# Optimization experiments

Hardware: AMD Instinct MI355X
Metric: run time of the kernel (lower is better)

Reference implementation:

```python
import jax, jax.numpy as jnp
import numpy as np

B, N, D, H, DK, DV, E = 32, 512, 128, 8, 16, 16, 128
MLP_H = 16


def _uniform(key, shape, fan):
    s = 1.0 / np.sqrt(fan)
    return jax.random.uniform(key, shape, jnp.float32, -s, s)


def setup_inputs() -> dict:
    key = jax.random.key(0)
    ks = jax.random.split(key, 13)
    q = jax.random.normal(ks[0], (B, N, D), jnp.float32)
    mask = jax.random.randint(ks[1], (B, N, N), 0, 2) > 0  # True = attention not allowed
    edge_matrix = jax.random.normal(ks[2], (B, N, N), jnp.float32)
    # per-head projection weights (init: uniform(-1/sqrt(last_dim), ...))
    W_query = _uniform(ks[3], (H, D, DK), DK)
    W_key = _uniform(ks[4], (H, D, DK), DK)
    W_val = _uniform(ks[5], (H, D, DV), DV)
    W_out = _uniform(ks[6], (H, DV, E), E)
    # edge MLP: 1 -> 16 -> 16 -> n_heads, ReLU between layers
    mlp_W1 = _uniform(ks[7], (1, MLP_H), 1)
    mlp_b1 = _uniform(ks[8], (MLP_H,), 1)
    mlp_W2 = _uniform(ks[9], (MLP_H, MLP_H), MLP_H)
    mlp_b2 = _uniform(ks[10], (MLP_H,), MLP_H)
    mlp_W3 = _uniform(ks[11], (MLP_H, H), MLP_H)
    mlp_b3 = _uniform(ks[12], (H,), MLP_H)
    return dict(q=q, mask=mask, edge_matrix=edge_matrix,
                W_query=W_query, W_key=W_key, W_val=W_val, W_out=W_out,
                mlp_W1=mlp_W1, mlp_b1=mlp_b1, mlp_W2=mlp_W2, mlp_b2=mlp_b2,
                mlp_W3=mlp_W3, mlp_b3=mlp_b3)


def reference(q, mask, edge_matrix, W_query, W_key, W_val, W_out,
              mlp_W1, mlp_b1, mlp_W2, mlp_b2, mlp_W3, mlp_b3):
    dk = W_query.shape[-1]
    norm = 1.0 / np.sqrt(dk)
    # per-head projections: [H,B,N,dk]
    Q = jnp.einsum('bni,hid->hbnd', q, W_query)
    K = jnp.einsum('bni,hid->hbnd', q, W_key)
    V = jnp.einsum('bni,hid->hbnd', q, W_val)
    # scaled QK^T: [H,B,N,N]
    comp = norm * jnp.einsum('hbqd,hbkd->hbqk', Q, K)
    # edge-bias MLP on each scalar edge weight: [B,N,N,1] -> [B,N,N,H]
    e = edge_matrix[..., None]
    h1 = jax.nn.relu(e @ mlp_W1 + mlp_b1)
    h2 = jax.nn.relu(h1 @ mlp_W2 + mlp_b2)
    bias = h2 @ mlp_W3 + mlp_b3
    comp = comp + jnp.transpose(bias, (3, 0, 1, 2))
    # masked softmax (mask True = disallowed)
    m = mask[None]  # broadcast over heads
    comp = jnp.where(m, -jnp.inf, comp)
    attn = jax.nn.softmax(comp, axis=-1)
    attn = jnp.where(m, 0.0, attn)
    heads = jnp.einsum('hbqk,hbkd->hbqd', attn, V)  # [H,B,N,dv]
    out = jnp.einsum('hbqd,hde->bqe', heads, W_out)  # [B,N,E]
    return out
```

## Files before the change

### kernel.cpp

```cpp
#include <hip/hip_runtime.h>
#include <hip/hip_bf16.h>
#include <float.h>

#define Bc 32
#define Nc 512
#define Dc 128
#define Hc 8
#define DKc 16
#define Ec 128
#define LOG2E 1.44269504088896340736f
#define SCLAMP 80.0f

typedef __attribute__((ext_vector_type(4))) short s16x4;
typedef __attribute__((ext_vector_type(8))) short s16x8;
typedef __attribute__((ext_vector_type(4))) float f32x4;

union BFU { __hip_bfloat16 b; short s; };
static __device__ inline short f2bf(float f) { BFU u; u.b = __float2bfloat16(f); return u.s; }

static __device__ inline unsigned rnd16(float x) { return __float_as_uint(x) + 0x8000u; }
static __device__ inline s16x4 pack4(float a, float b, float c, float d) {
  union { unsigned u[2]; s16x4 v; } r;
  r.u[0] = __builtin_amdgcn_perm(rnd16(b), rnd16(a), 0x07060302u);
  r.u[1] = __builtin_amdgcn_perm(rnd16(d), rnd16(c), 0x07060302u);
  return r.v;
}

#if __has_builtin(__builtin_amdgcn_exp2f)
#define EXP2F(x) __builtin_amdgcn_exp2f(x)
#else
#define EXP2F(x) exp2f(x)
#endif

static __device__ inline f32x4 mfma16(s16x4 a, s16x4 b, f32x4 c) {
#if __has_builtin(__builtin_amdgcn_mfma_f32_16x16x16bf16_1k)
  return __builtin_amdgcn_mfma_f32_16x16x16bf16_1k(a, b, c, 0, 0, 0);
#else
  int lane = threadIdx.x & 63;
  int g = lane >> 4, base = lane & 15;
  int src0 = (base + 32 * g) & 63;
  int src1 = (base + 32 * g + 16) & 63;
  int ax = ((int*)&a)[0], ay = ((int*)&a)[1];
  int bx = ((int*)&b)[0], by = ((int*)&b)[1];
  int A0 = __shfl(ax, src0), A1 = __shfl(ay, src0);
  int A2 = __shfl(ax, src1), A3 = __shfl(ay, src1);
  int B0 = __shfl(bx, src0), B1 = __shfl(by, src0);
  int B2 = __shfl(bx, src1), B3 = __shfl(by, src1);
  if (g >= 2) { A0 = A1 = A2 = A3 = 0; B0 = B1 = B2 = B3 = 0; }
  s16x8 A8, B8;
  ((int*)&A8)[0] = A0; ((int*)&A8)[1] = A1; ((int*)&A8)[2] = A2; ((int*)&A8)[3] = A3;
  ((int*)&B8)[0] = B0; ((int*)&B8)[1] = B1; ((int*)&B8)[2] = B2; ((int*)&B8)[3] = B3;
  return __builtin_amdgcn_mfma_f32_16x16x32_bf16(A8, B8, c, 0, 0, 0);
#endif
}

__global__ __launch_bounds__(256) void prep_kernel(
    const float* __restrict__ Wq, const float* __restrict__ Wk, const float* __restrict__ Wv,
    const float* __restrict__ Wo,
    const unsigned char* __restrict__ m, int* __restrict__ flag,
    short* __restrict__ Wt, short* __restrict__ Wob)
{
  int blk = blockIdx.x;
  int t = threadIdx.x;
  if (blk == 256) {
    __shared__ int red[4];
    int any = 0;
    for (int u = t; u < 16384; u += 256)
      if ((u & 3) != 0 && m[u] != 0) any = 1;
    unsigned long long bal = __ballot(any != 0);
    if ((t & 63) == 0) red[t >> 6] = (bal != 0ULL) ? 1 : 0;
    __syncthreads();
    if (t == 0) *flag = red[0] | red[1] | red[2] | red[3];
    return;
  }
  int o = blk * 256 + t;
  if (o < 49152) {
    int mat = o >> 14, r = o & 16383;
    int hk = r >> 7, d = r & 127;
    const float* src = (mat == 0) ? Wq : ((mat == 1) ? Wk : Wv);
    Wt[o] = f2bf(src[(hk >> 4) * 2048 + d * 16 + (hk & 15)]);
  } else {
    int o2 = o - 49152;
    int et = o2 >> 11, s = (o2 >> 8) & 7, lane = (o2 >> 2) & 63, i = o2 & 3;
    Wob[o2] = f2bf(Wo[(s * 16 + (lane >> 4) * 4 + i) * 128 + et * 16 + (lane & 15)]);
  }
}

__global__ __launch_bounds__(256, 4) void qkv4(
    const float* __restrict__ q, const short* __restrict__ Wt,
    short* __restrict__ Qb, short* __restrict__ Kb, short* __restrict__ Vt)
{
  __shared__ short qs[16][136];
  int blk = blockIdx.x;
  int b = blk >> 5;
  int rt = (blk & 31) << 4;
  int t = threadIdx.x;
  int wid = t >> 6, lane = t & 63;
  int lq = lane & 15, lg = lane >> 4;

  #pragma unroll
  for (int it = 0; it < 2; ++it) {
    int u = t + it * 256;
    int row = u >> 5, c4 = (u & 31) << 2;
    float4 v = *(const float4*)&q[((((b << 9) + rt + row) << 7)) + c4];
    *(s16x4*)&qs[row][c4] = pack4(v.x, v.y, v.z, v.w);
  }
  __syncthreads();

  s16x4 af[8];
  #pragma unroll
  for (int ks = 0; ks < 8; ++ks)
    af[ks] = *(const s16x4*)&qs[lq][ks * 16 + lg * 4];

  #pragma unroll 1
  for (int pj = 0; pj < 3; ++pj) {
    const short* Wm = Wt + pj * 16384;
    #pragma unroll
    for (int c2 = 0; c2 < 2; ++c2) {
      int ct = wid * 2 + c2;
      f32x4 acc = (f32x4)0.f;
      #pragma unroll
      for (int ks = 0; ks < 8; ++ks) {
        s16x4 bf = *(const s16x4*)&Wm[(ct * 16 + lq) * 128 + ks * 16 + lg * 4];
        acc = mfma16(af[ks], bf, acc);
      }
      if (pj == 0) {
        s16x4 pk = pack4(acc[0] * (0.25f * LOG2E), acc[1] * (0.25f * LOG2E),
                         acc[2] * (0.25f * LOG2E), acc[3] * (0.25f * LOG2E));
        #pragma unroll
        for (int r = 0; r < 4; ++r)
          Qb[(ct << 18) + (b << 13) + ((rt + lg * 4 + r) << 4) + lq] = pk[r];
      } else if (pj == 1) {
        s16x4 pk = pack4(acc[0], acc[1], acc[2], acc[3]);
        #pragma unroll
        for (int r = 0; r < 4; ++r)
          Kb[(ct << 18) + (b << 13) + ((rt + lg * 4 + r) << 4) + lq] = pk[r];
      } else {
        s16x4 pk = pack4(acc[0], acc[1], acc[2], acc[3]);
        *(s16x4*)&Vt[(ct << 18) + (((b << 4) + lq) << 9) + rt + lg * 4] = pk;
      }
    }
  }
}

__global__ __launch_bounds__(256, 4) void attn6(
    const float* __restrict__ edge, const unsigned char* __restrict__ maskB,
    const int* __restrict__ flag,
    const short* __restrict__ Qb, const short* __restrict__ Kb, const short* __restrict__ Vt,
    const short* __restrict__ Wob,
    const float* __restrict__ mW1, const float* __restrict__ mb1,
    const float* __restrict__ mW2, const float* __restrict__ mb2,
    const float* __restrict__ mW3, const float* __restrict__ mb3,
    float* __restrict__ out)
{
  __shared__ __align__(16) char smem[36864];

  int t = threadIdx.x;
  int wid = t >> 6, lane = t & 63;
  int lq = lane & 15, lg = lane >> 4;
  int b = blockIdx.x >> 5;
  int qt = (blockIdx.x & 31) << 4;
  int mflag = *flag;

  short* bias_w = (short*)(smem + wid * 5120);
  float (*etile)[16] = (float(*)[16])(smem + 20480 + wid * 1024);
  float* d2L = (float*)smem;
  float* psL = (float*)(smem + 34816);

  float W1v[4], b1v[4];
  f32x4 b2v, b3v;
  s16x4 w2f, w3f;
  #pragma unroll
  for (int i = 0; i < 4; ++i) {
    int v = lg * 4 + i;
    W1v[i] = mW1[v];
    b1v[i] = mb1[v];
    b2v[i] = mb2[v];
    b3v[i] = (v < 8) ? mb3[v] * LOG2E : 0.f;
    w2f[i] = f2bf(mW2[v * 16 + lq]);
    w3f[i] = (lq < 8) ? f2bf(mW3[v * 8 + lq] * LOG2E) : (short)0;
  }

  const short* Kl = Kb + (b << 13) + (lq << 4) + (lg << 2);
  const short* Vl = Vt + (((b << 4) + lq) << 9) + (lg << 2);
  const short* Ql = Qb + (b << 13) + ((qt + lq) << 4) + (lg << 2);
  unsigned ebase = (((b << 9) + qt + (lane >> 2)) << 9) + (lane & 3) * 4;
  unsigned mbase = (((b << 9) + qt + lq) << 9) + (lg << 2);

  s16x4 qf[8];
  #pragma unroll
  for (int h = 0; h < 8; ++h) qf[h] = *(const s16x4*)(Ql + (h << 18));

  f32x4 oacc[8];
  float psum[8];
  #pragma unroll
  for (int h = 0; h < 8; ++h) { oacc[h] = (f32x4)0.f; psum[h] = 0.f; }

  int jb = wid << 4;
  float4 ev = *(const float4*)&edge[ebase + jb];
  int4 mkv;
  if (mflag) {
    uchar4 u = *(const uchar4*)&maskB[mbase + jb];
    mkv.x = u.x; mkv.y = u.y; mkv.z = u.z; mkv.w = u.w;
  } else {
    mkv = *(const int4*)&((const int*)maskB)[mbase + jb];
  }

  #pragma unroll 1
  for (int cc = 0; cc < 8; ++cc) {
    jb = ((cc << 2) | wid) << 4;
    *(float4*)&etile[lane >> 2][(lane & 3) * 4] = ev;

    float4 evn; int4 mkn;
    if (cc < 7) {
      int jbn = (((cc + 1) << 2) | wid) << 4;
      evn = *(const float4*)&edge[ebase + jbn];
      if (mflag) {
        uchar4 u = *(const uchar4*)&maskB[mbase + jbn];
        mkn.x = u.x; mkn.y = u.y; mkn.z = u.z; mkn.w = u.w;
      } else {
        mkn = *(const int4*)&((const int*)maskB)[mbase + jbn];
      }
    } else { evn = ev; mkn = mkv; }

    s16x4 kf[8];
    #pragma unroll
    for (int h = 0; h < 8; ++h) kf[h] = *(const s16x4*)(Kl + (h << 18) + (jb << 4));

    #pragma unroll 4
    for (int qq = 0; qq < 16; ++qq) {
      float e = etile[qq][lq];
      s16x4 h1f = pack4(fmaxf(0.f, fmaf(e, W1v[0], b1v[0])),
                        fmaxf(0.f, fmaf(e, W1v[1], b1v[1])),
                        fmaxf(0.f, fmaf(e, W1v[2], b1v[2])),
                        fmaxf(0.f, fmaf(e, W1v[3], b1v[3])));
      f32x4 c2 = mfma16(w2f, h1f, b2v);
      s16x4 rf = pack4(fmaxf(c2[0], 0.f), fmaxf(c2[1], 0.f),
                       fmaxf(c2[2], 0.f), fmaxf(c2[3], 0.f));
      f32x4 c3 = mfma16(w3f, rf, b3v);
      if (lg < 2) {
        s16x4 pk = pack4(c3[0], c3[1], c3[2], c3[3]);
        #pragma unroll
        for (int r = 0; r < 4; ++r)
          bias_w[(lg * 4 + r) * 320 + qq * 20 + lq] = pk[r];
      }
    }

    #pragma unroll
    for (int h = 0; h < 8; ++h) {
      union { s16x4 v; int i[2]; } bb;
      bb.v = *(const s16x4*)&bias_w[h * 320 + lq * 20 + lg * 4];
      f32x4 sc;
      sc[0] = __int_as_float(bb.i[0] << 16);
      sc[1] = __int_as_float(bb.i[0] & 0xffff0000);
      sc[2] = __int_as_float(bb.i[1] << 16);
      sc[3] = __int_as_float(bb.i[1] & 0xffff0000);
      sc = mfma16(kf[h], qf[h], sc);
      s16x4 vf = *(const s16x4*)(Vl + (h << 18) + jb);
      float p0 = mkv.x ? 0.f : EXP2F(fminf(sc[0], SCLAMP));
      float p1 = mkv.y ? 0.f : EXP2F(fminf(sc[1], SCLAMP));
      float p2 = mkv.z ? 0.f : EXP2F(fminf(sc[2], SCLAMP));
      float p3 = mkv.w ? 0.f : EXP2F(fminf(sc[3], SCLAMP));
      psum[h] += (p0 + p1) + (p2 + p3);
      s16x4 pf = pack4(p0, p1, p2, p3);
      oacc[h] = mfma16(vf, pf, oacc[h]);
    }
    ev = evn; mkv = mkn;
  }

  #pragma unroll
  for (int h = 0; h < 8; ++h) {
    float s = psum[h];
    s += __shfl_xor(s, 16);
    s += __shfl_xor(s, 32);
    psum[h] = s;
  }
  if (lg == 0) {
    #pragma unroll
    for (int h = 0; h < 8; ++h) psL[wid * 128 + h * 16 + lq] = psum[h];
  }
  __syncthreads();

  s16x4 obf[8];
  #pragma unroll
  for (int h = 0; h < 8; ++h) {
    float tot = psL[h * 16 + lq] + psL[128 + h * 16 + lq]
              + psL[256 + h * 16 + lq] + psL[384 + h * 16 + lq];
    float inv = (tot > 0.f) ? 1.f / tot : 0.f;
    obf[h] = pack4(oacc[h][0] * inv, oacc[h][1] * inv, oacc[h][2] * inv, oacc[h][3] * inv);
  }

  f32x4 d2a[8];
  #pragma unroll
  for (int et = 0; et < 8; ++et) d2a[et] = (f32x4)0.f;
  #pragma unroll
  for (int s = 0; s < 8; ++s) {
    #pragma unroll
    for (int et = 0; et < 8; ++et) {
      s16x4 wo = *(const s16x4*)&Wob[((et * 8 + s) << 8) + (lane << 2)];
      d2a[et] = mfma16(wo, obf[s], d2a[et]);
    }
  }

  #pragma unroll
  for (int et = 0; et < 8; ++et)
    #pragma unroll
    for (int r = 0; r < 4; ++r)
      d2L[(wid * 128 + et * 16 + lg * 4 + r) * 17 + lq] = d2a[et][r];
  __syncthreads();

  #pragma unroll
  for (int k = 0; k < 2; ++k) {
    int et = wid * 2 + k;
    #pragma unroll
    for (int r = 0; r < 4; ++r) {
      int el = (et * 16 + lg * 4 + r) * 17 + lq;
      float v = d2L[el] + d2L[2176 + el] + d2L[4352 + el] + d2L[6528 + el];
      out[(((b << 9) + qt + lq) << 7) + et * 16 + lg * 4 + r] = v;
    }
  }
}

extern "C" void kernel_launch(void* const* d_in, const int* in_sizes, int n_in,
                              void* d_out, int out_size, void* d_ws, size_t ws_size,
                              hipStream_t stream)
{
  const float* q    = (const float*)d_in[0];
  const unsigned char* mask = (const unsigned char*)d_in[1];
  const float* edge = (const float*)d_in[2];
  const float* Wq   = (const float*)d_in[3];
  const float* Wk   = (const float*)d_in[4];
  const float* Wv   = (const float*)d_in[5];
  const float* Wo   = (const float*)d_in[6];
  const float* mW1  = (const float*)d_in[7];
  const float* mb1  = (const float*)d_in[8];
  const float* mW2  = (const float*)d_in[9];
  const float* mb2  = (const float*)d_in[10];
  const float* mW3  = (const float*)d_in[11];
  const float* mb3  = (const float*)d_in[12];
  float* out = (float*)d_out;

  size_t per = (size_t)Hc * Bc * Nc * DKc;
  short* Wt  = (short*)d_ws;
  short* Wob = Wt + 49152;
  short* Qb  = Wob + 16384;
  short* Kb  = Qb + per;
  short* Vt  = Kb + per;
  int* flag  = (int*)(Vt + per);

  prep_kernel<<<dim3(257), dim3(256), 0, stream>>>(Wq, Wk, Wv, Wo, mask, flag, Wt, Wob);
  qkv4<<<dim3(Bc * 32), dim3(256), 0, stream>>>(q, Wt, Qb, Kb, Vt);
  attn6<<<dim3(Bc * 32), dim3(256), 0, stream>>>(edge, mask, flag, Qb, Kb, Vt, Wob,
      mW1, mb1, mW2, mb2, mW3, mb3, out);
}
```

Baseline: 124.2 us.

## Replace per-element edge MLP with exact piecewise-linear lookup table

The scalar-input ReLU edge MLP is an exact piecewise-linear function of the edge weight. A new prep block finds its breakpoints (first-layer and second-layer ReLU knots), sorts them, and stores a slope and intercept per segment and head. The attention kernel now copies this table into shared memory, binary-searches each edge value's segment, and gets each head's bias with one FMA, replacing the per-tile MFMA-based MLP evaluation and its bias staging in shared memory. The trade-off is dependent shared-memory lookups with scattered access patterns, and pack4 now uses a library bf16 conversion instead of the manual bit-twiddling path.

```diff
diff --git a/kernel.cpp b/kernel.cpp
--- a/kernel.cpp
+++ b/kernel.cpp
@@ -10,6 +10,7 @@
 #define Ec 128
 #define LOG2E 1.44269504088896340736f
 #define SCLAMP 80.0f
+#define KPAD 3.0e38f
 
 typedef __attribute__((ext_vector_type(4))) short s16x4;
 typedef __attribute__((ext_vector_type(8))) short s16x8;
@@ -17,13 +18,8 @@
 
 union BFU { __hip_bfloat16 b; short s; };
 static __device__ inline short f2bf(float f) { BFU u; u.b = __float2bfloat16(f); return u.s; }
-
-static __device__ inline unsigned rnd16(float x) { return __float_as_uint(x) + 0x8000u; }
 static __device__ inline s16x4 pack4(float a, float b, float c, float d) {
-  union { unsigned u[2]; s16x4 v; } r;
-  r.u[0] = __builtin_amdgcn_perm(rnd16(b), rnd16(a), 0x07060302u);
-  r.u[1] = __builtin_amdgcn_perm(rnd16(d), rnd16(c), 0x07060302u);
-  return r.v;
+  s16x4 r; r[0] = f2bf(a); r[1] = f2bf(b); r[2] = f2bf(c); r[3] = f2bf(d); return r;
 }
 
 #if __has_builtin(__builtin_amdgcn_exp2f)
@@ -54,14 +50,49 @@
 #endif
 }
 
+static __device__ __forceinline__ void h2pre_eval(
+    float e, const float* W1, const float* B1, const float* W2, const float* B2,
+    float* h2)
+{
+  float h1[16];
+  #pragma unroll
+  for (int u = 0; u < 16; ++u) h1[u] = fmaxf(0.f, fmaf(e, W1[u], B1[u]));
+  #pragma unroll
+  for (int v = 0; v < 16; ++v) {
+    float a = B2[v];
+    #pragma unroll
+    for (int u = 0; u < 16; ++u) a = fmaf(h1[u], W2[u * 16 + v], a);
+    h2[v] = a;
+  }
+}
+static __device__ __forceinline__ void bias_eval(
+    float e, const float* W1, const float* B1, const float* W2, const float* B2,
+    const float* W3, const float* B3, float* bias8)
+{
+  float h2[16];
+  h2pre_eval(e, W1, B1, W2, B2, h2);
+  #pragma unroll
+  for (int h = 0; h < 8; ++h) {
+    float a = B3[h];
+    #pragma unroll
+    for (int v = 0; v < 16; ++v) a = fmaf(fmaxf(h2[v], 0.f), W3[v * 8 + h], a);
+    bias8[h] = a;
+  }
+}
+
 __global__ __launch_bounds__(256) void prep_kernel(
     const float* __restrict__ Wq, const float* __restrict__ Wk, const float* __restrict__ Wv,
     const float* __restrict__ Wo,
     const unsigned char* __restrict__ m, int* __restrict__ flag,
-    short* __restrict__ Wt, short* __restrict__ Wob)
+    short* __restrict__ Wt, short* __restrict__ Wob,
+    const float* __restrict__ mW1, const float* __restrict__ mb1,
+    const float* __restrict__ mW2, const float* __restrict__ mb2,
+    const float* __restrict__ mW3, const float* __restrict__ mb3,
+    float* __restrict__ knotsG, float* __restrict__ coeffG)
 {
   int blk = blockIdx.x;
   int t = threadIdx.x;
+
   if (blk == 256) {
     __shared__ int red[4];
     int any = 0;
@@ -73,6 +104,111 @@
     if (t == 0) *flag = red[0] | red[1] | red[2] | red[3];
     return;
   }
+
+  if (blk == 257) {
+    __shared__ float t1raw[16], t1s[16];
+    __shared__ float ks[512], ks2[512];
+    __shared__ int cnt, n1s;
+
+    if (t < 16) {
+      float w = mW1[t];
+      t1raw[t] = (w != 0.f) ? (-mb1[t] / w) : KPAD;
+    }
+    for (int u = t; u < 512; u += 256) { ks[u] = KPAD; ks2[u] = KPAD; }
+    __syncthreads();
+    if (t < 16) {
+      float v = t1raw[t];
+      int r = 0;
+      #pragma unroll
+      for (int j = 0; j < 16; ++j) {
+        float vj = t1raw[j];
+        r += (vj < v) || (vj == v && j < t);
+      }
+      t1s[r] = v;
+    }
+    __syncthreads();
+    if (t == 0) {
+      int n1 = 0;
+      while (n1 < 16 && t1s[n1] < 1.0e37f) { ks[n1] = t1s[n1]; n1++; }
+      n1s = n1;
+      cnt = n1;
+    }
+    __syncthreads();
+    int n1 = n1s;
+    if (t <= n1) {
+      bool first = (t == 0), last = (t == n1);
+      float L = first ? 0.f : t1s[t - 1];
+      float R = last ? 0.f : t1s[t];
+      float p1, p2;
+      bool ok = true;
+      if (first && last) { p1 = 0.f; p2 = 1.f; }
+      else if (first)    { p1 = R - 1.f; p2 = R - 0.5f; }
+      else if (last)     { p1 = L + 0.5f; p2 = L + 1.f; }
+      else {
+        float w = R - L;
+        if (w > 0.f) { p1 = L + 0.25f * w; p2 = L + 0.75f * w; }
+        else ok = false;
+      }
+      if (ok && p2 > p1) {
+        float h2a[16], h2b[16];
+        h2pre_eval(p1, mW1, mb1, mW2, mb2, h2a);
+        h2pre_eval(p2, mW1, mb1, mW2, mb2, h2b);
+        #pragma unroll
+        for (int v = 0; v < 16; ++v) {
+          float bet = (h2b[v] - h2a[v]) / (p2 - p1);
+          float alp = fmaf(-bet, p1, h2a[v]);
+          float x = -alp / bet;
+          bool fin = (x == x) && (fabsf(x) < 1.0e37f) && (bet != 0.f);
+          bool inr = (first || x > L) && (last || x < R);
+          if (fin && inr) { int id = atomicAdd(&cnt, 1); ks[id] = x; }
+        }
+      }
+    }
+    __syncthreads();
+    int mknots = cnt;
+    for (int i = t; i < mknots; i += 256) {
+      float v = ks[i];
+      int r = 0;
+      for (int j = 0; j < mknots; ++j) {
+        float vj = ks[j];
+        r += (vj < v) || (vj == v && j < i);
+      }
+      ks2[r] = v;
+    }
+    __syncthreads();
+    for (int u = t; u < 512; u += 256) knotsG[u] = ks2[u];
+    for (int s = t; s < mknots + 1; s += 256) {
+      bool first = (s == 0), last = (s == mknots);
+      float L = first ? 0.f : ks2[s - 1];
+      float R = last ? 0.f : ks2[s];
+      float p1, p2;
+      if (first && last) { p1 = 0.f; p2 = 1.f; }
+      else if (first)    { p1 = R - 1.f; p2 = R - 0.5f; }
+      else if (last)     { p1 = L + 0.5f; p2 = L + 1.f; }
+      else { float w = R - L; p1 = L + 0.25f * w; p2 = L + 0.75f * w; }
+      float ba[8];
+      bias_eval(p1, mW1, mb1, mW2, mb2, mW3, mb3, ba);
+      if (p2 > p1) {
+        float bb[8];
+        bias_eval(p2, mW1, mb1, mW2, mb2, mW3, mb3, bb);
+        #pragma unroll
+        for (int h = 0; h < 8; ++h) {
+          float sl = (bb[h] - ba[h]) / (p2 - p1);
+          float c0 = fmaf(-sl, p1, ba[h]);
+          coeffG[h * 640 + s * 2]     = sl * LOG2E;
+          coeffG[h * 640 + s * 2 + 1] = c0 * LOG2E;
+        }
+      } else {
+        #pragma unroll
+        for (int h = 0; h < 8; ++h) {
+          coeffG[h * 640 + s * 2]     = 0.f;
+          coeffG[h * 640 + s * 2 + 1] = ba[h] * LOG2E;
+        }
+      }
+    }
+    return;
+  }
+
   int o = blk * 256 + t;
   if (o < 49152) {
     int mat = o >> 14, r = o & 16383;
@@ -143,14 +279,20 @@
   }
 }
 
-__global__ __launch_bounds__(256, 4) void attn6(
+static __device__ __forceinline__ int segof(const float* knotsL, float e) {
+  int p = 0;
+  #pragma unroll
+  for (int s = 256; s > 0; s >>= 1)
+    p += (knotsL[p + s - 1] <= e) ? s : 0;
+  return p;
+}
+
+__global__ __launch_bounds__(256, 4) void attn7(
     const float* __restrict__ edge, const unsigned char* __restrict__ maskB,
     const int* __restrict__ flag,
     const short* __restrict__ Qb, const short* __restrict__ Kb, const short* __restrict__ Vt,
     const short* __restrict__ Wob,
-    const float* __restrict__ mW1, const float* __restrict__ mb1,
-    const float* __restrict__ mW2, const float* __restrict__ mb2,
-    const float* __restrict__ mW3, const float* __restrict__ mb3,
+    const float* __restrict__ knotsG, const float* __restrict__ coeffG,
     float* __restrict__ out)
 {
   __shared__ __align__(16) char smem[36864];
@@ -162,29 +304,17 @@
   int qt = (blockIdx.x & 31) << 4;
   int mflag = *flag;
 
-  short* bias_w = (short*)(smem + wid * 5120);
-  float (*etile)[16] = (float(*)[16])(smem + 20480 + wid * 1024);
+  float* knotsL = (float*)smem;
+  float* coeffL = (float*)(smem + 2048);
   float* d2L = (float*)smem;
   float* psL = (float*)(smem + 34816);
 
-  float W1v[4], b1v[4];
-  f32x4 b2v, b3v;
-  s16x4 w2f, w3f;
-  #pragma unroll
-  for (int i = 0; i < 4; ++i) {
-    int v = lg * 4 + i;
-    W1v[i] = mW1[v];
-    b1v[i] = mb1[v];
-    b2v[i] = mb2[v];
-    b3v[i] = (v < 8) ? mb3[v] * LOG2E : 0.f;
-    w2f[i] = f2bf(mW2[v * 16 + lq]);
-    w3f[i] = (lq < 8) ? f2bf(mW3[v * 8 + lq] * LOG2E) : (short)0;
-  }
+  for (int u = t; u < 1408; u += 256)
+    ((float4*)smem)[u] = ((const float4*)knotsG)[u];
 
   const short* Kl = Kb + (b << 13) + (lq << 4) + (lg << 2);
   const short* Vl = Vt + (((b << 4) + lq) << 9) + (lg << 2);
   const short* Ql = Qb + (b << 13) + ((qt + lq) << 4) + (lg << 2);
-  unsigned ebase = (((b << 9) + qt + (lane >> 2)) << 9) + (lane & 3) * 4;
   unsigned mbase = (((b << 9) + qt + lq) << 9) + (lg << 2);
 
   s16x4 qf[8];
@@ -197,7 +327,7 @@
   for (int h = 0; h < 8; ++h) { oacc[h] = (f32x4)0.f; psum[h] = 0.f; }
 
   int jb = wid << 4;
-  float4 ev = *(const float4*)&edge[ebase + jb];
+  float4 ev = *(const float4*)&edge[mbase + jb];
   int4 mkv;
   if (mflag) {
     uchar4 u = *(const uchar4*)&maskB[mbase + jb];
@@ -206,15 +336,16 @@
     mkv = *(const int4*)&((const int*)maskB)[mbase + jb];
   }
 
+  __syncthreads();
+
   #pragma unroll 1
   for (int cc = 0; cc < 8; ++cc) {
     jb = ((cc << 2) | wid) << 4;
-    *(float4*)&etile[lane >> 2][(lane & 3) * 4] = ev;
 
     float4 evn; int4 mkn;
     if (cc < 7) {
       int jbn = (((cc + 1) << 2) | wid) << 4;
-      evn = *(const float4*)&edge[ebase + jbn];
+      evn = *(const float4*)&edge[mbase + jbn];
       if (mflag) {
         uchar4 u = *(const uchar4*)&maskB[mbase + jbn];
         mkn.x = u.x; mkn.y = u.y; mkn.z = u.z; mkn.w = u.w;
@@ -227,34 +358,27 @@
     #pragma unroll
     for (int h = 0; h < 8; ++h) kf[h] = *(const s16x4*)(Kl + (h << 18) + (jb << 4));
 
-    #pragma unroll 4
-    for (int qq = 0; qq < 16; ++qq) {
-      float e = etile[qq][lq];
-      s16x4 h1f = pack4(fmaxf(0.f, fmaf(e, W1v[0], b1v[0])),
-                        fmaxf(0.f, fmaf(e, W1v[1], b1v[1])),
-                        fmaxf(0.f, fmaf(e, W1v[2], b1v[2])),
-                        fmaxf(0.f, fmaf(e, W1v[3], b1v[3])));
-      f32x4 c2 = mfma16(w2f, h1f, b2v);
-      s16x4 rf = pack4(fmaxf(c2[0], 0.f), fmaxf(c2[1], 0.f),
-                       fmaxf(c2[2], 0.f), fmaxf(c2[3], 0.f));
-      f32x4 c3 = mfma16(w3f, rf, b3v);
-      if (lg < 2) {
-        s16x4 pk = pack4(c3[0], c3[1], c3[2], c3[3]);
-        #pragma unroll
-        for (int r = 0; r < 4; ++r)
-          bias_w[(lg * 4 + r) * 320 + qq * 20 + lq] = pk[r];
-      }
-    }
+    int sg0 = segof(knotsL, ev.x);
+    int sg1 = segof(knotsL, ev.y);
+    int sg2 = segof(knotsL, ev.z);
+    int sg3 = segof(knotsL, ev.w);
+    const float* c0 = coeffL + (sg0 << 1);
+    const float* c1 = coeffL + (sg1 << 1);
+    const float* c2 = coeffL + (sg2 << 1);
+    const float* c3 = coeffL + (sg3 << 1);
 
     #pragma unroll
     for (int h = 0; h < 8; ++h) {
-      union { s16x4 v; int i[2]; } bb;
-      bb.v = *(const s16x4*)&bias_w[h * 320 + lq * 20 + lg * 4];
+      int hb = h * 640;
+      float2 a0 = *(const float2*)(c0 + hb);
+      float2 a1 = *(const float2*)(c1 + hb);
+      float2 a2 = *(const float2*)(c2 + hb);
+      float2 a3 = *(const float2*)(c3 + hb);
       f32x4 sc;
-      sc[0] = __int_as_float(bb.i[0] << 16);
-      sc[1] = __int_as_float(bb.i[0] & 0xffff0000);
-      sc[2] = __int_as_float(bb.i[1] << 16);
-      sc[3] = __int_as_float(bb.i[1] & 0xffff0000);
+      sc[0] = fmaf(a0.x, ev.x, a0.y);
+      sc[1] = fmaf(a1.x, ev.y, a1.y);
+      sc[2] = fmaf(a2.x, ev.z, a2.y);
+      sc[3] = fmaf(a3.x, ev.w, a3.y);
       sc = mfma16(kf[h], qf[h], sc);
       s16x4 vf = *(const s16x4*)(Vl + (h << 18) + jb);
       float p0 = mkv.x ? 0.f : EXP2F(fminf(sc[0], SCLAMP));
@@ -346,10 +470,13 @@
   short* Qb  = Wob + 16384;
   short* Kb  = Qb + per;
   short* Vt  = Kb + per;
-  int* flag  = (int*)(Vt + per);
-
-  prep_kernel<<<dim3(257), dim3(256), 0, stream>>>(Wq, Wk, Wv, Wo, mask, flag, Wt, Wob);
+  float* knotsG = (float*)(Vt + per);
+  float* coeffG = knotsG + 512;
+  int* flag  = (int*)(coeffG + 5120);
+
+  prep_kernel<<<dim3(258), dim3(256), 0, stream>>>(Wq, Wk, Wv, Wo, mask, flag, Wt, Wob,
+      mW1, mb1, mW2, mb2, mW3, mb3, knotsG, coeffG);
   qkv4<<<dim3(Bc * 32), dim3(256), 0, stream>>>(q, Wt, Qb, Kb, Vt);
-  attn6<<<dim3(Bc * 32), dim3(256), 0, stream>>>(edge, mask, flag, Qb, Kb, Vt, Wob,
-      mW1, mb1, mW2, mb2, mW3, mb3, out);
-}
+  attn7<<<dim3(Bc * 32), dim3(256), 0, stream>>>(edge, mask, flag, Qb, Kb, Vt, Wob,
+      knotsG, coeffG, out);
+}
```

After: 141.6 us. +13.9%, slower.
